# Performance work log

Hardware: AMD Instinct MI355X
Metric: run time of the kernel (lower is better)

Reference implementation:

```python
import jax, jax.numpy as jnp
import numpy as np

N_NODES = 100000
N_EDGES = 1600000
D = 128
L = 3
D_OUT = 64


def setup_inputs() -> dict:
    key = jax.random.key(0)
    ks = jax.random.split(key, 6)
    x = jax.random.normal(ks[0], (N_NODES, D), dtype=jnp.float32)
    edge_index = jax.random.randint(ks[1], (2, N_EDGES), 0, N_NODES, dtype=jnp.int64)
    # Kaiming-ish init scale for linear layers
    s = 1.0 / np.sqrt(D)
    W_rel = jax.random.normal(ks[2], (L, D, D), dtype=jnp.float32) * s
    b_rel = jnp.zeros((L, D), dtype=jnp.float32)
    W_root = jax.random.normal(ks[3], (L, D, D), dtype=jnp.float32) * s
    fc_w = jax.random.normal(ks[4], (D_OUT, D), dtype=jnp.float32) * s
    fc_b = jnp.zeros((D_OUT,), dtype=jnp.float32)
    return {"x": x, "edge_index": edge_index, "W_rel": W_rel, "b_rel": b_rel,
            "W_root": W_root, "fc_w": fc_w, "fc_b": fc_b}


def reference(x, edge_index, W_rel, b_rel, W_root, fc_w, fc_b):
    # PyG GraphConv (aggr='add'): x_i' = W_root x_i + W_rel * sum_{j in N(i)} x_j + b
    src, dst = edge_index[0], edge_index[1]
    n = x.shape[0]
    num_layers = W_rel.shape[0]  # static small loop over layers
    for l in range(num_layers):
        agg = jax.ops.segment_sum(x[src], dst, num_segments=n)  # [N, D] scatter-add of gathered neighbor feats
        x = agg @ W_rel[l].T + b_rel[l] + x @ W_root[l].T
    return x @ fc_w.T + fc_b
```

## Files before the change

### kernel.cpp

```cpp
#include <hip/hip_runtime.h>


typedef short bf16x8 __attribute__((ext_vector_type(8)));
typedef float f32x4 __attribute__((ext_vector_type(4)));

#define CAPB 8192

__device__ inline float bf2f(unsigned short u) {
    union { unsigned int i; float f; } v; v.i = ((unsigned int)u) << 16; return v.f;
}
__device__ inline unsigned short f2bf(float f) {
    union { float f; unsigned int i; } v; v.f = f;
    unsigned int r = v.i + 0x7FFFu + ((v.i >> 16) & 1u);
    return (unsigned short)(r >> 16);
}

__global__ __launch_bounds__(512) void prep_kernel(
    const float* __restrict__ Wr2, const float* __restrict__ Wo2,
    const float* __restrict__ fcw, float* __restrict__ K0_2, float* __restrict__ K1_2,
    const int* __restrict__ src, const int* __restrict__ dst,
    int* __restrict__ gcur, unsigned int* __restrict__ bucketed, int e, int NA, int NB) {
    int b = blockIdx.x, t = threadIdx.x;
    if (b < 64) {
        if (t < 256) {
            int matid = b >> 5;
            const float* W = matid ? Wr2 : Wo2;
            float* K = matid ? K1_2 : K0_2;
            int i = t & 127;
            int j = (b & 31) * 2 + (t >> 7);
            float acc = 0.f;
            for (int k = 0; k < 128; k++) acc += W[k * 128 + i] * fcw[j * 128 + k];
            K[i * 64 + j] = acc;
        }
        return;
    }
    b -= 64;
    if (b < NA) {
        __shared__ int sHist[512], sScan[512], sExcl[512], sGbase[512];
        __shared__ unsigned int lbuf[2048];
        __shared__ unsigned short lbkt[2048];
        int e0 = b * 2048;
        int cnt = e - e0; if (cnt > 2048) cnt = 2048;
        sHist[t] = 0;
        __syncthreads();
        unsigned int pk[4]; int bk[4];
#pragma unroll
        for (int k = 0; k < 4; k++) {
            int j = t + k * 512;
            if (j < cnt) {
                int d = dst[e0 + j], s = src[e0 + j];
                bk[k] = d >> 8;
                pk[k] = ((unsigned int)s << 8) | (unsigned int)(d & 255);
                atomicAdd(&sHist[bk[k]], 1);
            } else bk[k] = -1;
        }
        __syncthreads();
        int h = sHist[t];
        if (t < NB && h > 0) sGbase[t] = atomicAdd(&gcur[t], h);
        else sGbase[t] = 0;
        int xv = h; sScan[t] = xv; __syncthreads();
        for (int o = 1; o < 512; o <<= 1) {
            int y = (t >= o) ? sScan[t - o] : 0;
            __syncthreads();
            xv += y; sScan[t] = xv;
            __syncthreads();
        }
        sExcl[t] = xv - h;
        sHist[t] = 0;
        __syncthreads();
#pragma unroll
        for (int k = 0; k < 4; k++) {
            if (bk[k] >= 0) {
                int r = atomicAdd(&sHist[bk[k]], 1);
                int pos = sExcl[bk[k]] + r;
                lbuf[pos] = pk[k];
                lbkt[pos] = (unsigned short)bk[k];
            }
        }
        __syncthreads();
        for (int j = t; j < cnt; j += 512) {
            int b2 = lbkt[j];
            int idx = sGbase[b2] + (j - sExcl[b2]);
            if (idx < CAPB) bucketed[(size_t)b2 * CAPB + idx] = lbuf[j];
        }
    }
}

__global__ __launch_bounds__(256) void partB_kernel(
    const unsigned int* __restrict__ bucketed, const int* __restrict__ gcur,
    int* __restrict__ deg, int* __restrict__ start, int* __restrict__ csr, int n) {
    int b = blockIdx.x, t = threadIdx.x;
    __shared__ int ldeg[256], lscan[256], red[256];
    __shared__ int csr_base_s;
    int cnt = gcur[b]; if (cnt > CAPB) cnt = CAPB;
    int part = 0;
    for (int q = t; q < b; q += 256) { int c = gcur[q]; part += (c > CAPB ? CAPB : c); }
    red[t] = part; __syncthreads();
    for (int o = 128; o > 0; o >>= 1) { if (t < o) red[t] += red[t + o]; __syncthreads(); }
    if (t == 0) csr_base_s = red[0];
    ldeg[t] = 0;
    __syncthreads();
    const unsigned int* bd = bucketed + (size_t)b * CAPB;
    for (int j = t; j < cnt; j += 256) atomicAdd(&ldeg[bd[j] & 255], 1);
    __syncthreads();
    int h = ldeg[t];
    int xv = h; lscan[t] = xv; __syncthreads();
    for (int o = 1; o < 256; o <<= 1) {
        int y = (t >= o) ? lscan[t - o] : 0;
        __syncthreads();
        xv += y; lscan[t] = xv;
        __syncthreads();
    }
    int excl = xv - h;
    int csr_base = csr_base_s;
    int node = b * 256 + t;
    if (node < n) { deg[node] = h; start[node] = csr_base + excl; }
    __syncthreads();
    lscan[t] = excl;
    ldeg[t] = 0;
    __syncthreads();
    for (int j = t; j < cnt; j += 256) {
        unsigned int pkd = bd[j];
        int d = pkd & 255;
        int r = atomicAdd(&ldeg[d], 1);
        csr[csr_base + lscan[d] + r] = (int)(pkd >> 8);
    }
}

__global__ __launch_bounds__(256) void stage2_kernel(
    const float* __restrict__ Wr1, const float* __restrict__ Wo1,
    const float* __restrict__ K0_2, const float* __restrict__ K1_2,
    float* __restrict__ K0_1, float* __restrict__ K1_1, float* __restrict__ K2_1) {
    int b = blockIdx.x, t = threadIdx.x;
    int matid = b >> 5;
    int i = t & 127;
    int j = (b & 31) * 2 + (t >> 7);
    float acc = 0.f;
    if (matid == 0) {
        for (int k = 0; k < 128; k++) acc += Wo1[k * 128 + i] * K0_2[k * 64 + j];
        K0_1[i * 64 + j] = acc;
    } else if (matid == 1) {
        for (int k = 0; k < 128; k++)
            acc += Wr1[k * 128 + i] * K0_2[k * 64 + j] + Wo1[k * 128 + i] * K1_2[k * 64 + j];
        K1_1[i * 64 + j] = acc;
    } else {
        for (int k = 0; k < 128; k++) acc += Wr1[k * 128 + i] * K1_2[k * 64 + j];
        K2_1[i * 64 + j] = acc;
    }
}

__global__ __launch_bounds__(256) void stage3_kernel(
    const float* __restrict__ Wr0, const float* __restrict__ Wo0,
    const float* __restrict__ K0_1, const float* __restrict__ K1_1, const float* __restrict__ K2_1,
    const float* __restrict__ K0_2, const float* __restrict__ K1_2,
    const float* __restrict__ br, const float* __restrict__ fcw, const float* __restrict__ fcb,
    unsigned short* __restrict__ Nw, float* __restrict__ Bv) {
    int b = blockIdx.x, t = threadIdx.x;
    if (b < 128) {
        int matid = b >> 5;
        int i = t & 127;
        int o = (b & 31) * 2 + (t >> 7);
        float acc = 0.f;
        if (matid == 0) {
            for (int k = 0; k < 128; k++) acc += Wo0[k * 128 + i] * K0_1[k * 64 + o];
        } else if (matid == 1) {
            for (int k = 0; k < 128; k++)
                acc += Wr0[k * 128 + i] * K0_1[k * 64 + o] + Wo0[k * 128 + i] * K1_1[k * 64 + o];
        } else if (matid == 2) {
            for (int k = 0; k < 128; k++)
                acc += Wr0[k * 128 + i] * K1_1[k * 64 + o] + Wo0[k * 128 + i] * K2_1[k * 64 + o];
        } else {
            for (int k = 0; k < 128; k++) acc += Wr0[k * 128 + i] * K2_1[k * 64 + o];
        }
        int p = ((o & 3) << 4) | (o >> 2);
        Nw[p * 512 + matid * 128 + i] = f2bf(acc);
        return;
    }
    const float* br0 = br;
    const float* br1 = br + 128;
    const float* br2 = br + 256;
    int j = t & 63;
    int which = t >> 6;
    if (which == 0) {
        float acc = fcb[j];
        for (int k = 0; k < 128; k++) acc += br2[k] * fcw[j * 128 + k];
        for (int k = 0; k < 128; k++) acc += br1[k] * K0_2[k * 64 + j];
        for (int k = 0; k < 128; k++) acc += br0[k] * K0_1[k * 64 + j];
        Bv[j] = acc;
    } else if (which == 1) {
        float acc = 0.f;
        for (int k = 0; k < 128; k++) acc += br1[k] * K1_2[k * 64 + j];
        for (int k = 0; k < 128; k++) acc += br0[k] * K1_1[k * 64 + j];
        Bv[64 + j] = acc;
    } else if (which == 2) {
        float acc = 0.f;
        for (int k = 0; k < 128; k++) acc += br0[k] * K2_1[k * 64 + j];
        Bv[128 + j] = acc;
    }
}

__global__ __launch_bounds__(256, 4) void gemm_u_kernel(
    const float* __restrict__ x, const unsigned short* __restrict__ Nw,
    unsigned short* __restrict__ U, int n) {
    int matid = threadIdx.x >> 6;
    int lane = threadIdx.x & 63;
    int m    = lane & 15;
    int quad = lane >> 4;
    size_t n64 = (size_t)n * 64;
    unsigned short* up = U + (size_t)matid * n64;

    bf16x8 b[4][4];
#pragma unroll
    for (int t = 0; t < 4; t++)
#pragma unroll
        for (int kk = 0; kk < 4; kk++)
            b[t][kk] = *(const bf16x8*)(Nw + (size_t)(t * 16 + m) * 512 + matid * 128 + kk * 32 + quad * 8);
#pragma unroll
    for (int t = 0; t < 4; t++)
#pragma unroll
        for (int kk = 0; kk < 4; kk++)
            asm volatile("" : "+v"(b[t][kk]));

    const int base_tile = blockIdx.x * 4;

#pragma unroll
    for (int it = 0; it < 4; it++) {
        int row0 = (base_tile + it) * 16;

        int arow = row0 + m; if (arow >= n) arow = n - 1;
        const float* xr = x + (size_t)arow * 128 + quad * 8;
        bf16x8 a[4];
#pragma unroll
        for (int kk = 0; kk < 4; kk++) {
            float4 v0 = *(const float4*)(xr + kk * 32);
            float4 v1 = *(const float4*)(xr + kk * 32 + 4);
            a[kk][0] = (short)f2bf(v0.x); a[kk][1] = (short)f2bf(v0.y);
            a[kk][2] = (short)f2bf(v0.z); a[kk][3] = (short)f2bf(v0.w);
            a[kk][4] = (short)f2bf(v1.x); a[kk][5] = (short)f2bf(v1.y);
            a[kk][6] = (short)f2bf(v1.z); a[kk][7] = (short)f2bf(v1.w);
        }

        f32x4 acc[4];
#pragma unroll
        for (int t = 0; t < 4; t++) acc[t] = (f32x4){0.f, 0.f, 0.f, 0.f};
#pragma unroll
        for (int kk = 0; kk < 4; kk++)
#pragma unroll
            for (int t = 0; t < 4; t++)
                acc[t] = __builtin_amdgcn_mfma_f32_16x16x32_bf16(a[kk], b[t][kk], acc[t], 0, 0, 0);

#pragma unroll
        for (int r = 0; r < 4; r++) {
            int orow = row0 + quad * 4 + r;
            if (orow < n) {
                ushort4 o4;
                o4.x = f2bf(acc[0][r]); o4.y = f2bf(acc[1][r]);
                o4.z = f2bf(acc[2][r]); o4.w = f2bf(acc[3][r]);
                *(ushort4*)(up + (size_t)orow * 64 + m * 4) = o4;
            }
        }
    }
}

template <int MODE>
__global__ __launch_bounds__(256) void agg64_kernel(
    const unsigned short* __restrict__ in, const unsigned short* __restrict__ addv,
    const int* __restrict__ csr, const int* __restrict__ start, const int* __restrict__ deg,
    unsigned short* __restrict__ outb, float* __restrict__ outf,
    const float* __restrict__ Bv, int* __restrict__ d2w, const int* __restrict__ d2r, int n) {
    int tid = threadIdx.x;
    int fl  = tid & 7;
    int node = blockIdx.x * 32 + (tid >> 3);
    if (node >= n) return;

    float b0[8], b1[8], b2[8];
    if (MODE == 2) {
#pragma unroll
        for (int j = 0; j < 8; j++) {
            int o = fl * 8 + j;
            b0[j] = Bv[o]; b1[j] = Bv[64 + o]; b2[j] = Bv[128 + o];
        }
    }

    int s0 = start[node];
    int d  = deg[node];

    float acc[8];
#pragma unroll
    for (int j = 0; j < 8; j++) acc[j] = 0.f;
    int dsum = 0;

#pragma unroll 4
    for (int i = 0; i < d; i++) {
        int s = csr[s0 + i];
        bf16x8 v = *(const bf16x8*)(in + (size_t)s * 64 + fl * 8);
#pragma unroll
        for (int j = 0; j < 8; j++) acc[j] += bf2f((unsigned short)v[j]);
        if (MODE == 0 && fl == 0) dsum += deg[s];
    }
    if (MODE == 0 && fl == 0) d2w[node] = dsum;

    bf16x8 av = *(const bf16x8*)(addv + (size_t)node * 64 + fl * 8);
    if (MODE < 2) {
        bf16x8 o;
#pragma unroll
        for (int j = 0; j < 8; j++) o[j] = (short)f2bf(acc[j] + bf2f((unsigned short)av[j]));
        *(bf16x8*)(outb + (size_t)node * 64 + fl * 8) = o;
    } else {
        float dg = (float)d;
        float dd = (float)d2r[node];
        float ov[8];
#pragma unroll
        for (int j = 0; j < 8; j++)
            ov[j] = acc[j] + bf2f((unsigned short)av[j]) + b0[j] + dg * b1[j] + dd * b2[j];
        float* op = outf + (size_t)node * 64 + fl * 8;
        *(float4*)(op)     = make_float4(ov[0], ov[1], ov[2], ov[3]);
        *(float4*)(op + 4) = make_float4(ov[4], ov[5], ov[6], ov[7]);
    }
}

extern "C" void kernel_launch(void* const* d_in, const int* in_sizes, int n_in,
                              void* d_out, int out_size, void* d_ws, size_t ws_size,
                              hipStream_t stream) {
    const float* x      = (const float*)d_in[0];
    const int*   ei     = (const int*)d_in[1];
    const float* W_rel  = (const float*)d_in[2];
    const float* b_rel  = (const float*)d_in[3];
    const float* W_root = (const float*)d_in[4];
    const float* fc_w   = (const float*)d_in[5];
    const float* fc_b   = (const float*)d_in[6];

    const int n = in_sizes[0] / 128;
    const int e = in_sizes[1] / 2;
    const int* src = ei;
    const int* dst = ei + e;

    const int NB  = (n + 255) >> 8;
    const int NA  = (e + 2047) / 2048;
    const int NT  = (n + 15) / 16;
    const int NGB = (NT + 3) / 4;

    char* p = (char*)d_ws;
    auto take = [&](size_t bytes) -> void* {
        void* r = (void*)p;
        p += (bytes + 255) & ~(size_t)255;
        return r;
    };
    unsigned short* U  = (unsigned short*)take((size_t)n * 256 * 2);
    unsigned short* w1 = (unsigned short*)take((size_t)n * 64 * 2);
    unsigned short* w2 = (unsigned short*)take((size_t)n * 64 * 2);
    int* deg    = (int*)take((size_t)n * 4);
    int* start  = (int*)take((size_t)n * 4);
    int* d2     = (int*)take((size_t)n * 4);
    int* csr    = (int*)take((size_t)e * 4);
    unsigned int* bucketed = (unsigned int*)take((size_t)NB * CAPB * 4);
    int* gcur   = (int*)take((size_t)NB * 4);
    float* K0_2 = (float*)take(128 * 64 * 4);
    float* K1_2 = (float*)take(128 * 64 * 4);
    float* K0_1 = (float*)take(128 * 64 * 4);
    float* K1_1 = (float*)take(128 * 64 * 4);
    float* K2_1 = (float*)take(128 * 64 * 4);
    unsigned short* Nw = (unsigned short*)take(64 * 512 * 2);
    float* Bv   = (float*)take(192 * 4);

    size_t n64 = (size_t)n * 64;
    unsigned short* u0 = U;
    unsigned short* u1 = U + n64;
    unsigned short* u2 = U + 2 * n64;
    unsigned short* u3 = U + 3 * n64;

    hipMemsetAsync(gcur, 0, (size_t)NB * 4, stream);
    prep_kernel<<<64 + NA, 512, 0, stream>>>(
        W_rel + 2 * 16384, W_root + 2 * 16384, fc_w, K0_2, K1_2,
        src, dst, gcur, bucketed, e, NA, NB);
    partB_kernel<<<NB, 256, 0, stream>>>(bucketed, gcur, deg, start, csr, n);
    stage2_kernel<<<96, 256, 0, stream>>>(
        W_rel + 16384, W_root + 16384, K0_2, K1_2, K0_1, K1_1, K2_1);
    stage3_kernel<<<129, 256, 0, stream>>>(
        W_rel, W_root, K0_1, K1_1, K2_1, K0_2, K1_2, b_rel, fc_w, fc_b, Nw, Bv);

    gemm_u_kernel<<<NGB, 256, 0, stream>>>(x, Nw, U, n);

    const int AGB = (n + 31) / 32;
    agg64_kernel<0><<<AGB, 256, 0, stream>>>(
        u3, u2, csr, start, deg, w1, nullptr, nullptr, d2, nullptr, n);
    agg64_kernel<1><<<AGB, 256, 0, stream>>>(
        w1, u1, csr, start, deg, w2, nullptr, nullptr, nullptr, nullptr, n);
    agg64_kernel<2><<<AGB, 256, 0, stream>>>(
        w2, u0, csr, start, deg, nullptr, (float*)d_out, Bv, nullptr, d2, n);
}
```

Baseline: 337.7 us.

## Stage weight tiles in LDS and split gemm_u blocks by output matrix

The U projection kernel now assigns one output matrix per block rather than one per wave. It stages that matrix's 64x128 bf16 weight slice into shared memory once per block and reads B fragments from LDS inside the MFMA loop, instead of holding all of them in registers. Each wave now handles two 16-row tiles, and the occupancy hint rises from 4 to 6. This cuts register pressure and raises occupancy, but each x row is now read by four different blocks instead of one, and LDS reads are added to the inner loop.

```diff
diff --git a/kernel.cpp b/kernel.cpp
--- a/kernel.cpp
+++ b/kernel.cpp
@@ -199,33 +199,36 @@
     }
 }
 
-__global__ __launch_bounds__(256, 4) void gemm_u_kernel(
+__global__ __launch_bounds__(256, 6) void gemm_u_kernel(
     const float* __restrict__ x, const unsigned short* __restrict__ Nw,
     unsigned short* __restrict__ U, int n) {
-    int matid = threadIdx.x >> 6;
-    int lane = threadIdx.x & 63;
+    __shared__ unsigned short Blds[8192];
+    int matid = blockIdx.x & 3;
+    int blk   = blockIdx.x >> 2;
+    int tid   = threadIdx.x;
+
+    {
+        const uint4* nw4 = (const uint4*)Nw;
+        uint4* lds4 = (uint4*)Blds;
+        for (int g = tid; g < 1024; g += 256) {
+            int slot = g & 63;
+            int kq   = g >> 6;
+            lds4[g] = nw4[(size_t)slot * 64 + matid * 16 + kq];
+        }
+    }
+    __syncthreads();
+
+    int wave = tid >> 6;
+    int lane = tid & 63;
     int m    = lane & 15;
     int quad = lane >> 4;
     size_t n64 = (size_t)n * 64;
     unsigned short* up = U + (size_t)matid * n64;
 
-    bf16x8 b[4][4];
-#pragma unroll
-    for (int t = 0; t < 4; t++)
-#pragma unroll
-        for (int kk = 0; kk < 4; kk++)
-            b[t][kk] = *(const bf16x8*)(Nw + (size_t)(t * 16 + m) * 512 + matid * 128 + kk * 32 + quad * 8);
-#pragma unroll
-    for (int t = 0; t < 4; t++)
-#pragma unroll
-        for (int kk = 0; kk < 4; kk++)
-            asm volatile("" : "+v"(b[t][kk]));
-
-    const int base_tile = blockIdx.x * 4;
-
-#pragma unroll
-    for (int it = 0; it < 4; it++) {
-        int row0 = (base_tile + it) * 16;
+#pragma unroll
+    for (int w = 0; w < 2; w++) {
+        int row0 = (blk * 8 + wave * 2 + w) * 16;
+        if (row0 >= n) break;
 
         int arow = row0 + m; if (arow >= n) arow = n - 1;
         const float* xr = x + (size_t)arow * 128 + quad * 8;
@@ -244,10 +247,15 @@
 #pragma unroll
         for (int t = 0; t < 4; t++) acc[t] = (f32x4){0.f, 0.f, 0.f, 0.f};
 #pragma unroll
-        for (int kk = 0; kk < 4; kk++)
+        for (int kk = 0; kk < 4; kk++) {
+            bf16x8 bq[4];
 #pragma unroll
             for (int t = 0; t < 4; t++)
-                acc[t] = __builtin_amdgcn_mfma_f32_16x16x32_bf16(a[kk], b[t][kk], acc[t], 0, 0, 0);
+                bq[t] = *(const bf16x8*)(Blds + ((kk * 4 + quad) * 64 + t * 16 + m) * 8);
+#pragma unroll
+            for (int t = 0; t < 4; t++)
+                acc[t] = __builtin_amdgcn_mfma_f32_16x16x32_bf16(a[kk], bq[t], acc[t], 0, 0, 0);
+        }
 
 #pragma unroll
         for (int r = 0; r < 4; r++) {
@@ -338,7 +346,7 @@
     const int NB  = (n + 255) >> 8;
     const int NA  = (e + 2047) / 2048;
     const int NT  = (n + 15) / 16;
-    const int NGB = (NT + 3) / 4;
+    const int NGB = (NT + 7) / 8;
 
     char* p = (char*)d_ws;
     auto take = [&](size_t bytes) -> void* {
@@ -379,7 +387,7 @@
     stage3_kernel<<<129, 256, 0, stream>>>(
         W_rel, W_root, K0_1, K1_1, K2_1, K0_2, K1_2, b_rel, fc_w, fc_b, Nw, Bv);
 
-    gemm_u_kernel<<<NGB, 256, 0, stream>>>(x, Nw, U, n);
+    gemm_u_kernel<<<NGB * 4, 256, 0, stream>>>(x, Nw, U, n);
 
     const int AGB = (n + 31) / 32;
     agg64_kernel<0><<<AGB, 256, 0, stream>>>(
```

Result: slower. 348.7 us (+3.2%).
